# Performance work log

Measured on AMD Instinct MI355X. Metric: run time of the kernel, lower is better.

## Reference

```python
import jax, jax.numpy as jnp
import numpy as np

KERNELS = ("gaussian", "laplacian", "gaussian", "laplacian")
N, M, D, N_PER = 384, 384, 64, 200


def setup_inputs():
    key = jax.random.key(0)
    kx, ky, kb, kp = jax.random.split(key, 4)
    X = jax.random.normal(kx, (N, D), dtype=jnp.float32)
    Y = jax.random.normal(ky, (M, D), dtype=jnp.float32)
    # positive bandwidths of realistic magnitude for d=64 gaussian/laplacian kernels
    bandwidths = jax.random.uniform(kb, (4,), dtype=jnp.float32) * 8.0 + 4.0
    # each row is a random permutation of n+m indices (torch.randperm equivalent)
    perms = jax.vmap(lambda k: jax.random.permutation(k, N + M))(
        jax.random.split(kp, N_PER)).astype(jnp.int32)
    return {"X": X, "Y": Y, "bandwidths": bandwidths, "perms": perms}


def _pairwise_dist(Z):
    # torch.cdist(Z, Z, p=2); eps keeps sqrt grad finite on the zero diagonal
    sq = jnp.sum(Z * Z, axis=1)
    d2 = jnp.maximum(sq[:, None] + sq[None, :] - 2.0 * (Z @ Z.T), 0.0)
    return jnp.sqrt(d2 + 1e-12)


def reference(X, Y, bandwidths, perms):
    n, m = X.shape[0], Y.shape[0]
    Z = jnp.concatenate([X, Y], axis=0)            # [n+m, d]
    dist = _pairwise_dist(Z)                        # [n+m, n+m]
    idx = jnp.arange(min(n, m))
    perm_X, perm_Y = perms[:, :n], perms[:, n:]    # [n_per, n], [n_per, m]
    U, U_b = [], []
    for i, kern in enumerate(KERNELS):
        b = bandwidths[i]
        if kern == "gaussian":
            K = jnp.exp(-(dist * dist) / (b * b))
        else:  # laplacian
            K = jnp.exp(-dist / b)
        # mmd_u's in-place K_XY[diag]=0 mutates the view of K, so zero first
        K = K.at[idx, n + idx].set(0.0)
        K_XX, K_YY, K_XY = K[:n, :n], K[n:, n:], K[:n, n:]
        mmd = ((K_XX.sum() - jnp.trace(K_XX)) / (n * (n - 1))
               + (K_YY.sum() - jnp.trace(K_YY)) / (m * (m - 1))
               - 2.0 * K_XY.sum() / (n * m))
        U.append(mmd)
        # fast_perm: gather permuted blocks, zero diagonals, reduce per permutation
        diagK = jnp.diagonal(K)
        sXX = K[perm_X[:, :, None], perm_X[:, None, :]].sum((1, 2)) - diagK[perm_X].sum(1)
        sYY = K[perm_Y[:, :, None], perm_Y[:, None, :]].sum((1, 2)) - diagK[perm_Y].sum(1)
        sXY = (K[perm_X[:, :, None], perm_Y[:, None, :]].sum((1, 2))
               - K[perm_X[:, idx], perm_Y[:, idx]].sum(1))
        U_b.append(sXX / (n * (n - 1)) + sYY / (m * (m - 1)) - 2.0 * sXY / (n * m))
    U = jnp.stack(U)[:, None]    # [n_b, 1]  == compute_U_stats U.unsqueeze(1)
    U_b = jnp.stack(U_b)         # [n_b, n_per]
    return jnp.concatenate([U, U_b], axis=1)  # [n_b, 1 + n_per]
```

## Files before the change

kernel.cpp:

```cpp
#include <hip/hip_runtime.h>

#define NTOT 768
#define NHALF 384
#define DDIM 64
#define NPER 200
#define PPAD 256
#define NKER 4
#define CHUNK 192
#define NMB 12
#define NNC 8

typedef __attribute__((ext_vector_type(8))) short short8;
typedef __attribute__((ext_vector_type(4))) float floatx4;

constexpr int K0SZ  = NTOT * NTOT;
constexpr int OF_KH = 0;
constexpr int KH_FLOATS = NKER * K0SZ / 2;
constexpr int OF_RS0 = OF_KH + KH_FLOATS;
constexpr int OF_RSX = OF_RS0 + NKER * NTOT;
constexpr int OF_RSY = OF_RSX + NKER * NTOT;
constexpr int OF_C   = OF_RSY + NKER * NTOT;
constexpr int OF_ROWM = OF_C + NKER * NHALF;
constexpr int OF_COLM = OF_ROWM + NKER * NTOT;
constexpr int OF_SCAL = OF_COLM + NKER * NTOT;
constexpr int OF_STT  = OF_SCAL + 16;
constexpr int STT_FLOATS = PPAD * NTOT / 2;
constexpr int OF_Q0P  = OF_STT + STT_FLOATS;

__device__ __forceinline__ unsigned short f2bf(float f) {
    unsigned int u = __float_as_uint(f);
    return (unsigned short)((u + 0x7FFFu + ((u >> 16) & 1u)) >> 16);
}
__device__ __forceinline__ float bf2f(unsigned short h) {
    return __uint_as_float(((unsigned int)h) << 16);
}

__global__ __launch_bounds__(256) void k_stage1(const float* __restrict__ X,
                                                const float* __restrict__ Y,
                                                const float* __restrict__ bw,
                                                const int* __restrict__ perms,
                                                float* __restrict__ ws) {
    __shared__ float zb[CHUNK * 65];
    __shared__ float zaS[DDIM];
    __shared__ float redw[32];
    int bid = blockIdx.x, tid = threadIdx.x;
    unsigned short* STT = (unsigned short*)(ws + OF_STT);

    if (bid < NPER) {
        if (tid < 192) {
            ((uint2*)(STT + bid * NTOT))[tid] = make_uint2(0u, 0u);
            if (bid < PPAD - NPER)
                ((uint2*)(STT + (NPER + bid) * NTOT))[tid] = make_uint2(0u, 0u);
        }
        __syncthreads();
        int v = perms[bid * NTOT + tid];
        STT[bid * NTOT + v] = 0x3F80;
        if (tid < NHALF - 256) {
            int v2 = perms[bid * NTOT + 256 + tid];
            STT[bid * NTOT + v2] = 0x3F80;
        }
        return;
    }

    int a = bid - NPER;
    unsigned short* KH = (unsigned short*)(ws + OF_KH);
    const float* za = (a < NHALF) ? X + a * DDIM : Y + (a - NHALF) * DDIM;
    if (tid < DDIM) zaS[tid] = za[tid];
    float ib2[NKER], ib1[NKER];
#pragma unroll
    for (int k = 0; k < NKER; ++k) { float b = bw[k]; ib2[k] = 1.f / (b * b); ib1[k] = 1.f / b; }
    __syncthreads();
    float sqa = 0.f;
#pragma unroll
    for (int d = 0; d < DDIM; ++d) sqa = fmaf(zaS[d], zaS[d], sqa);

    float accX[NKER] = {0.f, 0.f, 0.f, 0.f};
    float accY[NKER] = {0.f, 0.f, 0.f, 0.f};

    for (int c0 = 0; c0 < NTOT; c0 += CHUNK) {
        __syncthreads();
        for (int idx = tid; idx < CHUNK * DDIM; idx += 256) {
            int r = idx >> 6, d = idx & 63;
            int gr = c0 + r;
            const float* zr = (gr < NHALF) ? X + gr * DDIM : Y + (gr - NHALF) * DDIM;
            zb[r * 65 + d] = zr[d];
        }
        __syncthreads();
        if (tid < CHUNK) {
            int b = c0 + tid;
            float dot = 0.f, sqb = 0.f;
#pragma unroll
            for (int d = 0; d < DDIM; ++d) {
                float zv = zb[tid * 65 + d];
                dot = fmaf(zaS[d], zv, dot);
                sqb = fmaf(zv, zv, sqb);
            }
            float d2 = (sqa + sqb) - 2.f * dot;
            if (b == a) d2 = 0.f;
            d2 = fmaxf(d2, 0.f);
            float d2e = d2 + 1e-12f;
            float dist = sqrtf(d2e);
#pragma unroll
            for (int k = 0; k < NKER; ++k) {
                float val = ((k & 1) == 0) ? __expf(-d2e * ib2[k]) : __expf(-dist * ib1[k]);
                KH[k * K0SZ + a * NTOT + b] = f2bf(val);
                if (b < NHALF) accX[k] += val; else accY[k] += val;
                if (a < NHALF && b == a + NHALF) ws[OF_C + k * NHALF + a] = val;
            }
        }
    }
    float vals[8];
#pragma unroll
    for (int k = 0; k < NKER; ++k) { vals[k] = accX[k]; vals[4 + k] = accY[k]; }
#pragma unroll
    for (int off = 32; off > 0; off >>= 1)
#pragma unroll
        for (int v = 0; v < 8; ++v) vals[v] += __shfl_down(vals[v], off, 64);
    int wid = tid >> 6, lane = tid & 63;
    if (lane == 0)
#pragma unroll
        for (int v = 0; v < 8; ++v) redw[wid * 8 + v] = vals[v];
    __syncthreads();
    if (tid == 0) {
#pragma unroll
        for (int k = 0; k < NKER; ++k) {
            float sx = redw[k] + redw[8 + k] + redw[16 + k] + redw[24 + k];
            float sy = redw[4 + k] + redw[12 + k] + redw[20 + k] + redw[28 + k];
            ws[OF_RS0 + k * NTOT + a] = sx + sy;
            ws[OF_RSX + k * NTOT + a] = sx;
            ws[OF_RSY + k * NTOT + a] = sy;
        }
    }
}

__global__ __launch_bounds__(256) void k_stage2(const float* __restrict__ bw,
                                                float* __restrict__ ws,
                                                float* __restrict__ out) {
    __shared__ float shred[128];
    int bid = blockIdx.x, tid = threadIdx.x;

    if (bid < NMB * NNC * NKER) {
        int mb = bid % NMB;
        int t  = bid / NMB;
        int nc = t % NNC;
        int k  = t / NNC;
        int wave = tid >> 6, lane = tid & 63;
        int m0 = mb * 64 + wave * 16;
        int n0 = nc * 32;
        int row = lane & 15, quad = lane >> 4;
        const unsigned short* KH  = (const unsigned short*)(ws + OF_KH);
        const unsigned short* STT = (const unsigned short*)(ws + OF_STT);
        const unsigned short* aptr = KH + k * K0SZ + (m0 + row) * NTOT + quad * 8;
        const unsigned short* b0p  = STT + (n0 + row) * NTOT + quad * 8;
        const unsigned short* b1p  = STT + (n0 + 16 + row) * NTOT + quad * 8;
        floatx4 acc00 = {0.f,0.f,0.f,0.f}, acc01 = {0.f,0.f,0.f,0.f};
        floatx4 acc10 = {0.f,0.f,0.f,0.f}, acc11 = {0.f,0.f,0.f,0.f};
        for (int kk = 0; kk < NTOT; kk += 64) {
            short8 a0  = *(const short8*)(aptr + kk);
            short8 a1  = *(const short8*)(aptr + kk + 32);
            short8 b00 = *(const short8*)(b0p + kk);
            short8 b01 = *(const short8*)(b0p + kk + 32);
            short8 b10 = *(const short8*)(b1p + kk);
            short8 b11 = *(const short8*)(b1p + kk + 32);
            acc00 = __builtin_amdgcn_mfma_f32_16x16x32_bf16(a0, b00, acc00, 0, 0, 0);
            acc01 = __builtin_amdgcn_mfma_f32_16x16x32_bf16(a1, b01, acc01, 0, 0, 0);
            acc10 = __builtin_amdgcn_mfma_f32_16x16x32_bf16(a0, b10, acc10, 0, 0, 0);
            acc11 = __builtin_amdgcn_mfma_f32_16x16x32_bf16(a1, b11, acc11, 0, 0, 0);
        }
        const unsigned short* s0 = STT + (n0 + row) * NTOT + m0 + quad * 4;
        const unsigned short* s1 = STT + (n0 + 16 + row) * NTOT + m0 + quad * 4;
        float p0 = 0.f, p1 = 0.f;
#pragma unroll
        for (int r = 0; r < 4; ++r) {
            p0 += (acc00[r] + acc01[r]) * bf2f(s0[r]);
            p1 += (acc10[r] + acc11[r]) * bf2f(s1[r]);
        }
        p0 += __shfl_down(p0, 32, 64); p0 += __shfl_down(p0, 16, 64);
        p1 += __shfl_down(p1, 32, 64); p1 += __shfl_down(p1, 16, 64);
        if (lane < 16) { shred[wave * 32 + lane] = p0; shred[wave * 32 + 16 + lane] = p1; }
        __syncthreads();
        if (tid < 32) {
            float s = shred[tid] + shred[32 + tid] + shred[64 + tid] + shred[96 + tid];
            ws[OF_Q0P + (k * NMB + mb) * PPAD + n0 + tid] = s;
        }
        return;
    }

    int k = bid - NMB * NNC * NKER;
    float v[5] = {0.f, 0.f, 0.f, 0.f, 0.f};
    for (int a = tid; a < NTOT; a += 256) v[0] += ws[OF_RS0 + k * NTOT + a];
    for (int a = tid; a < NHALF; a += 256) {
        v[1] += ws[OF_C + k * NHALF + a];
        v[2] += ws[OF_RSX + k * NTOT + a];
        v[3] += ws[OF_RSY + k * NTOT + NHALF + a];
        v[4] += ws[OF_RSY + k * NTOT + a];
    }
#pragma unroll
    for (int off = 32; off > 0; off >>= 1)
#pragma unroll
        for (int j = 0; j < 5; ++j) v[j] += __shfl_down(v[j], off, 64);
    int wid = tid >> 6, lane = tid & 63;
    if (lane == 0)
#pragma unroll
        for (int j = 0; j < 5; ++j) shred[wid * 8 + j] = v[j];
    __syncthreads();
    if (tid == 0) {
        float tot0 = shred[0] + shred[8] + shred[16] + shred[24];
        float csum = shred[1] + shred[9] + shred[17] + shred[25];
        float sxx  = shred[2] + shred[10] + shred[18] + shred[26];
        float syy  = shred[3] + shred[11] + shred[19] + shred[27];
        float sxy  = shred[4] + shred[12] + shred[20] + shred[28];
        float b = bw[k];
        float dist0 = sqrtf(1e-12f);
        float dk = ((k & 1) == 0) ? expf(-(dist0 * dist0) / (b * b)) : expf(-dist0 / b);
        ws[OF_SCAL + k * 4 + 0] = tot0 - csum;
        ws[OF_SCAL + k * 4 + 1] = dk;
        double U = ((double)sxx - 384.0 * (double)dk) * (1.0 / 147072.0)
                 + ((double)syy - 384.0 * (double)dk) * (1.0 / 147072.0)
                 - 2.0 * ((double)sxy - (double)csum) * (1.0 / 147456.0);
        out[k * 201] = (float)U;
    }
    for (int idx = tid; idx < NTOT; idx += 256) {
        float r0 = ws[OF_RS0 + k * NTOT + idx];
        float cx = (idx < NHALF)  ? ws[OF_C + k * NHALF + idx] : 0.f;
        float cy = (idx >= NHALF) ? ws[OF_C + k * NHALF + idx - NHALF] : 0.f;
        ws[OF_ROWM + k * NTOT + idx] = r0 - cx;
        ws[OF_COLM + k * NTOT + idx] = r0 - cy;
    }
}

__global__ __launch_bounds__(384) void k_perm(const int* __restrict__ perms,
                                              const float* __restrict__ ws,
                                              float* __restrict__ out) {
    int p = blockIdx.x, i = threadIdx.x;
    const unsigned short* STT = (const unsigned short*)(ws + OF_STT);
    const unsigned short* KH  = (const unsigned short*)(ws + OF_KH);
    int a  = perms[p * NTOT + i];
    int bY = perms[p * NTOT + NHALF + i];
    float si  = bf2f(STT[p * NTOT + i]);
    float si2 = bf2f(STT[p * NTOT + NHALF + i]);
    float v[16];
#pragma unroll
    for (int k = 0; k < NKER; ++k) {
        v[k * 4 + 0] = ws[OF_ROWM + k * NTOT + a];
        v[k * 4 + 1] = ws[OF_COLM + k * NTOT + a];
        float kv = bf2f(KH[k * K0SZ + a * NTOT + bY]);
        if (a < NHALF && bY == a + NHALF) kv = 0.f;
        v[k * 4 + 2] = kv;
        v[k * 4 + 3] = ws[OF_C + k * NHALF + i] * si * si2;
    }
#pragma unroll
    for (int off = 32; off > 0; off >>= 1)
#pragma unroll
        for (int j = 0; j < 16; ++j) v[j] += __shfl_down(v[j], off, 64);
    __shared__ float redw[6 * 16];
    int wid = i >> 6, lane = i & 63;
    if (lane == 0)
#pragma unroll
        for (int j = 0; j < 16; ++j) redw[wid * 16 + j] = v[j];
    __syncthreads();
    if (i < 16) {
        float s = 0.f;
#pragma unroll
        for (int w = 0; w < 6; ++w) s += redw[w * 16 + i];
        redw[i] = s;
    }
    __syncthreads();
    if (i < NKER) {
        int k = i;
        double rs = redw[k * 4 + 0], cs = redw[k * 4 + 1];
        double pair = redw[k * 4 + 2], qc = redw[k * 4 + 3];
        double total_mod = (double)ws[OF_SCAL + k * 4 + 0];
        double dk        = (double)ws[OF_SCAL + k * 4 + 1];
        double q = -qc;
#pragma unroll
        for (int mb = 0; mb < NMB; ++mb) q += (double)ws[OF_Q0P + (k * NMB + mb) * PPAD + p];
        double sXX = q - 384.0 * dk;
        double sYY = total_mod - rs - cs + q - 384.0 * dk;
        double sXY = rs - q - pair;
        out[k * 201 + 1 + p] =
            (float)(sXX * (1.0 / 147072.0) + sYY * (1.0 / 147072.0) - 2.0 * sXY * (1.0 / 147456.0));
    }
}

extern "C" void kernel_launch(void* const* d_in, const int* in_sizes, int n_in,
                              void* d_out, int out_size, void* d_ws, size_t ws_size,
                              hipStream_t stream) {
    const float* X     = (const float*)d_in[0];
    const float* Y     = (const float*)d_in[1];
    const float* bw    = (const float*)d_in[2];
    const int*   perms = (const int*)d_in[3];
    float* ws  = (float*)d_ws;
    float* out = (float*)d_out;

    k_stage1<<<NPER + NTOT, 256, 0, stream>>>(X, Y, bw, perms, ws);
    k_stage2<<<NMB * NNC * NKER + NKER, 256, 0, stream>>>(bw, ws, out);
    k_perm  <<<NPER, 384, 0, stream>>>(perms, ws, out);
}
```

Baseline: 107.1 us.

## Fuse three stages into one cooperative persistent kernel with grid syncs

Merges the three launches (distance/kernel matrix build, bf16 MFMA permutation GEMM, per-permutation reduction) into one cooperative kernel of 256 blocks that loops over work units and uses grid.sync between phases. The GEMM phase also now computes 64 permutation columns per block instead of 32, halving its block count and reusing each loaded A fragment across four B tiles. Phase C now uses 256 threads with a strided loop. The aim is to remove inter-kernel launch gaps and get more reuse in the GEMM. The cost is that only 256 blocks do the 968 phase-A units, and grid-wide barriers are added. A fallback to three separate launches remains if the cooperative launch fails.

```diff
diff --git a/kernel.cpp b/kernel.cpp
--- a/kernel.cpp
+++ b/kernel.cpp
@@ -1,4 +1,7 @@
 #include <hip/hip_runtime.h>
+#include <hip/hip_cooperative_groups.h>
+
+namespace cg = cooperative_groups;
 
 #define NTOT 768
 #define NHALF 384
@@ -8,7 +11,9 @@
 #define NKER 4
 #define CHUNK 192
 #define NMB 12
-#define NNC 8
+#define NBLK 256
+#define NB_GEMM 192
+#define NA_UNITS (NPER + NTOT)
 
 typedef __attribute__((ext_vector_type(8))) short short8;
 typedef __attribute__((ext_vector_type(4))) float floatx4;
@@ -27,6 +32,8 @@
 constexpr int STT_FLOATS = PPAD * NTOT / 2;
 constexpr int OF_Q0P  = OF_STT + STT_FLOATS;
 
+constexpr int SMEMF = CHUNK * 65 + DDIM + 32;
+
 __device__ __forceinline__ unsigned short f2bf(float f) {
     unsigned int u = __float_as_uint(f);
     return (unsigned short)((u + 0x7FFFu + ((u >> 16) & 1u)) >> 16);
@@ -35,45 +42,42 @@
     return __uint_as_float(((unsigned int)h) << 16);
 }
 
-__global__ __launch_bounds__(256) void k_stage1(const float* __restrict__ X,
-                                                const float* __restrict__ Y,
-                                                const float* __restrict__ bw,
-                                                const int* __restrict__ perms,
-                                                float* __restrict__ ws) {
-    __shared__ float zb[CHUNK * 65];
-    __shared__ float zaS[DDIM];
-    __shared__ float redw[32];
-    int bid = blockIdx.x, tid = threadIdx.x;
+__device__ __forceinline__ void phaseA_unit(int u, const float* __restrict__ X,
+                                            const float* __restrict__ Y,
+                                            const int* __restrict__ perms,
+                                            const float* ib2, const float* ib1,
+                                            float* __restrict__ ws, float* smem) {
+    int tid = threadIdx.x, wave = tid >> 6, lane = tid & 63;
+    float* zb  = smem;
+    float* zaS = smem + CHUNK * 65;
+    float* redw = smem + CHUNK * 65 + DDIM;
     unsigned short* STT = (unsigned short*)(ws + OF_STT);
-
-    if (bid < NPER) {
+    unsigned short* KH  = (unsigned short*)(ws + OF_KH);
+    __syncthreads();
+
+    if (u < NPER) {
         if (tid < 192) {
-            ((uint2*)(STT + bid * NTOT))[tid] = make_uint2(0u, 0u);
-            if (bid < PPAD - NPER)
-                ((uint2*)(STT + (NPER + bid) * NTOT))[tid] = make_uint2(0u, 0u);
+            ((uint2*)(STT + u * NTOT))[tid] = make_uint2(0u, 0u);
+            if (u < PPAD - NPER)
+                ((uint2*)(STT + (NPER + u) * NTOT))[tid] = make_uint2(0u, 0u);
         }
         __syncthreads();
-        int v = perms[bid * NTOT + tid];
-        STT[bid * NTOT + v] = 0x3F80;
+        int v = perms[u * NTOT + tid];
+        STT[u * NTOT + v] = 0x3F80;
         if (tid < NHALF - 256) {
-            int v2 = perms[bid * NTOT + 256 + tid];
-            STT[bid * NTOT + v2] = 0x3F80;
+            int v2 = perms[u * NTOT + 256 + tid];
+            STT[u * NTOT + v2] = 0x3F80;
         }
         return;
     }
 
-    int a = bid - NPER;
-    unsigned short* KH = (unsigned short*)(ws + OF_KH);
+    int a = u - NPER;
     const float* za = (a < NHALF) ? X + a * DDIM : Y + (a - NHALF) * DDIM;
     if (tid < DDIM) zaS[tid] = za[tid];
-    float ib2[NKER], ib1[NKER];
-#pragma unroll
-    for (int k = 0; k < NKER; ++k) { float b = bw[k]; ib2[k] = 1.f / (b * b); ib1[k] = 1.f / b; }
     __syncthreads();
     float sqa = 0.f;
 #pragma unroll
     for (int d = 0; d < DDIM; ++d) sqa = fmaf(zaS[d], zaS[d], sqa);
-
     float accX[NKER] = {0.f, 0.f, 0.f, 0.f};
     float accY[NKER] = {0.f, 0.f, 0.f, 0.f};
 
@@ -116,10 +120,10 @@
     for (int off = 32; off > 0; off >>= 1)
 #pragma unroll
         for (int v = 0; v < 8; ++v) vals[v] += __shfl_down(vals[v], off, 64);
-    int wid = tid >> 6, lane = tid & 63;
+    __syncthreads();
     if (lane == 0)
 #pragma unroll
-        for (int v = 0; v < 8; ++v) redw[wid * 8 + v] = vals[v];
+        for (int v = 0; v < 8; ++v) redw[wave * 8 + v] = vals[v];
     __syncthreads();
     if (tid == 0) {
 #pragma unroll
@@ -133,60 +137,57 @@
     }
 }
 
-__global__ __launch_bounds__(256) void k_stage2(const float* __restrict__ bw,
-                                                float* __restrict__ ws,
-                                                float* __restrict__ out) {
-    __shared__ float shred[128];
-    int bid = blockIdx.x, tid = threadIdx.x;
-
-    if (bid < NMB * NNC * NKER) {
-        int mb = bid % NMB;
-        int t  = bid / NMB;
-        int nc = t % NNC;
-        int k  = t / NNC;
-        int wave = tid >> 6, lane = tid & 63;
-        int m0 = mb * 64 + wave * 16;
-        int n0 = nc * 32;
-        int row = lane & 15, quad = lane >> 4;
-        const unsigned short* KH  = (const unsigned short*)(ws + OF_KH);
-        const unsigned short* STT = (const unsigned short*)(ws + OF_STT);
-        const unsigned short* aptr = KH + k * K0SZ + (m0 + row) * NTOT + quad * 8;
-        const unsigned short* b0p  = STT + (n0 + row) * NTOT + quad * 8;
-        const unsigned short* b1p  = STT + (n0 + 16 + row) * NTOT + quad * 8;
-        floatx4 acc00 = {0.f,0.f,0.f,0.f}, acc01 = {0.f,0.f,0.f,0.f};
-        floatx4 acc10 = {0.f,0.f,0.f,0.f}, acc11 = {0.f,0.f,0.f,0.f};
-        for (int kk = 0; kk < NTOT; kk += 64) {
-            short8 a0  = *(const short8*)(aptr + kk);
-            short8 a1  = *(const short8*)(aptr + kk + 32);
-            short8 b00 = *(const short8*)(b0p + kk);
-            short8 b01 = *(const short8*)(b0p + kk + 32);
-            short8 b10 = *(const short8*)(b1p + kk);
-            short8 b11 = *(const short8*)(b1p + kk + 32);
-            acc00 = __builtin_amdgcn_mfma_f32_16x16x32_bf16(a0, b00, acc00, 0, 0, 0);
-            acc01 = __builtin_amdgcn_mfma_f32_16x16x32_bf16(a1, b01, acc01, 0, 0, 0);
-            acc10 = __builtin_amdgcn_mfma_f32_16x16x32_bf16(a0, b10, acc10, 0, 0, 0);
-            acc11 = __builtin_amdgcn_mfma_f32_16x16x32_bf16(a1, b11, acc11, 0, 0, 0);
-        }
-        const unsigned short* s0 = STT + (n0 + row) * NTOT + m0 + quad * 4;
-        const unsigned short* s1 = STT + (n0 + 16 + row) * NTOT + m0 + quad * 4;
-        float p0 = 0.f, p1 = 0.f;
-#pragma unroll
-        for (int r = 0; r < 4; ++r) {
-            p0 += (acc00[r] + acc01[r]) * bf2f(s0[r]);
-            p1 += (acc10[r] + acc11[r]) * bf2f(s1[r]);
-        }
-        p0 += __shfl_down(p0, 32, 64); p0 += __shfl_down(p0, 16, 64);
-        p1 += __shfl_down(p1, 32, 64); p1 += __shfl_down(p1, 16, 64);
-        if (lane < 16) { shred[wave * 32 + lane] = p0; shred[wave * 32 + 16 + lane] = p1; }
-        __syncthreads();
-        if (tid < 32) {
-            float s = shred[tid] + shred[32 + tid] + shred[64 + tid] + shred[96 + tid];
-            ws[OF_Q0P + (k * NMB + mb) * PPAD + n0 + tid] = s;
-        }
-        return;
-    }
-
-    int k = bid - NMB * NNC * NKER;
+__device__ __forceinline__ void phaseB_gemm(int unit, float* __restrict__ ws, float* smem) {
+    int tid = threadIdx.x, wave = tid >> 6, lane = tid & 63;
+    int mb = unit % NMB;
+    int t  = unit / NMB;
+    int nc = t & 3;
+    int k  = t >> 2;
+    int m0 = mb * 64 + wave * 16;
+    int n0 = nc * 64;
+    int row = lane & 15, quad = lane >> 4;
+    const unsigned short* KH  = (const unsigned short*)(ws + OF_KH);
+    const unsigned short* STT = (const unsigned short*)(ws + OF_STT);
+    const unsigned short* aptr = KH + k * K0SZ + (m0 + row) * NTOT + quad * 8;
+    floatx4 acc[4][2];
+#pragma unroll
+    for (int j = 0; j < 4; ++j)
+#pragma unroll
+        for (int h = 0; h < 2; ++h) acc[j][h] = (floatx4){0.f, 0.f, 0.f, 0.f};
+    for (int kk = 0; kk < NTOT; kk += 64) {
+        short8 a0 = *(const short8*)(aptr + kk);
+        short8 a1 = *(const short8*)(aptr + kk + 32);
+#pragma unroll
+        for (int j = 0; j < 4; ++j) {
+            const unsigned short* bp = STT + (n0 + j * 16 + row) * NTOT + quad * 8 + kk;
+            short8 b0 = *(const short8*)(bp);
+            short8 b1 = *(const short8*)(bp + 32);
+            acc[j][0] = __builtin_amdgcn_mfma_f32_16x16x32_bf16(a0, b0, acc[j][0], 0, 0, 0);
+            acc[j][1] = __builtin_amdgcn_mfma_f32_16x16x32_bf16(a1, b1, acc[j][1], 0, 0, 0);
+        }
+    }
+    __syncthreads();
+#pragma unroll
+    for (int j = 0; j < 4; ++j) {
+        const unsigned short* sp = STT + (n0 + j * 16 + row) * NTOT + m0 + quad * 4;
+        float p = 0.f;
+#pragma unroll
+        for (int r = 0; r < 4; ++r) p += (acc[j][0][r] + acc[j][1][r]) * bf2f(sp[r]);
+        p += __shfl_down(p, 32, 64);
+        p += __shfl_down(p, 16, 64);
+        if (lane < 16) smem[wave * 64 + j * 16 + lane] = p;
+    }
+    __syncthreads();
+    if (tid < 64) {
+        float s = smem[tid] + smem[64 + tid] + smem[128 + tid] + smem[192 + tid];
+        ws[OF_Q0P + (k * NMB + mb) * PPAD + n0 + tid] = s;
+    }
+}
+
+__device__ __forceinline__ void phaseB_final(int k, const float* __restrict__ bw,
+                                             float* __restrict__ ws, float* __restrict__ out,
+                                             float* smem) {
+    int tid = threadIdx.x, wave = tid >> 6, lane = tid & 63;
     float v[5] = {0.f, 0.f, 0.f, 0.f, 0.f};
     for (int a = tid; a < NTOT; a += 256) v[0] += ws[OF_RS0 + k * NTOT + a];
     for (int a = tid; a < NHALF; a += 256) {
@@ -199,17 +200,17 @@
     for (int off = 32; off > 0; off >>= 1)
 #pragma unroll
         for (int j = 0; j < 5; ++j) v[j] += __shfl_down(v[j], off, 64);
-    int wid = tid >> 6, lane = tid & 63;
+    __syncthreads();
     if (lane == 0)
 #pragma unroll
-        for (int j = 0; j < 5; ++j) shred[wid * 8 + j] = v[j];
+        for (int j = 0; j < 5; ++j) smem[wave * 8 + j] = v[j];
     __syncthreads();
     if (tid == 0) {
-        float tot0 = shred[0] + shred[8] + shred[16] + shred[24];
-        float csum = shred[1] + shred[9] + shred[17] + shred[25];
-        float sxx  = shred[2] + shred[10] + shred[18] + shred[26];
-        float syy  = shred[3] + shred[11] + shred[19] + shred[27];
-        float sxy  = shred[4] + shred[12] + shred[20] + shred[28];
+        float tot0 = smem[0] + smem[8] + smem[16] + smem[24];
+        float csum = smem[1] + smem[9] + smem[17] + smem[25];
+        float sxx  = smem[2] + smem[10] + smem[18] + smem[26];
+        float syy  = smem[3] + smem[11] + smem[19] + smem[27];
+        float sxy  = smem[4] + smem[12] + smem[20] + smem[28];
         float b = bw[k];
         float dist0 = sqrtf(1e-12f);
         float dk = ((k & 1) == 0) ? expf(-(dist0 * dist0) / (b * b)) : expf(-dist0 / b);
@@ -229,47 +230,43 @@
     }
 }
 
-__global__ __launch_bounds__(384) void k_perm(const int* __restrict__ perms,
-                                              const float* __restrict__ ws,
-                                              float* __restrict__ out) {
-    int p = blockIdx.x, i = threadIdx.x;
+__device__ __forceinline__ void phaseC_unit(int p, const int* __restrict__ perms,
+                                            const float* __restrict__ ws,
+                                            float* __restrict__ out, float* smem) {
+    int tid = threadIdx.x, wave = tid >> 6, lane = tid & 63;
     const unsigned short* STT = (const unsigned short*)(ws + OF_STT);
     const unsigned short* KH  = (const unsigned short*)(ws + OF_KH);
-    int a  = perms[p * NTOT + i];
-    int bY = perms[p * NTOT + NHALF + i];
-    float si  = bf2f(STT[p * NTOT + i]);
-    float si2 = bf2f(STT[p * NTOT + NHALF + i]);
-    float v[16];
-#pragma unroll
-    for (int k = 0; k < NKER; ++k) {
-        v[k * 4 + 0] = ws[OF_ROWM + k * NTOT + a];
-        v[k * 4 + 1] = ws[OF_COLM + k * NTOT + a];
-        float kv = bf2f(KH[k * K0SZ + a * NTOT + bY]);
-        if (a < NHALF && bY == a + NHALF) kv = 0.f;
-        v[k * 4 + 2] = kv;
-        v[k * 4 + 3] = ws[OF_C + k * NHALF + i] * si * si2;
+    float v[16] = {0.f};
+    for (int i = tid; i < NHALF; i += 256) {
+        int a  = perms[p * NTOT + i];
+        int bY = perms[p * NTOT + NHALF + i];
+        float si  = bf2f(STT[p * NTOT + i]);
+        float si2 = bf2f(STT[p * NTOT + NHALF + i]);
+#pragma unroll
+        for (int k = 0; k < NKER; ++k) {
+            v[k * 4 + 0] += ws[OF_ROWM + k * NTOT + a];
+            v[k * 4 + 1] += ws[OF_COLM + k * NTOT + a];
+            float kv = bf2f(KH[k * K0SZ + a * NTOT + bY]);
+            if (a < NHALF && bY == a + NHALF) kv = 0.f;
+            v[k * 4 + 2] += kv;
+            v[k * 4 + 3] += ws[OF_C + k * NHALF + i] * si * si2;
+        }
     }
 #pragma unroll
     for (int off = 32; off > 0; off >>= 1)
 #pragma unroll
         for (int j = 0; j < 16; ++j) v[j] += __shfl_down(v[j], off, 64);
-    __shared__ float redw[6 * 16];
-    int wid = i >> 6, lane = i & 63;
+    __syncthreads();
     if (lane == 0)
 #pragma unroll
-        for (int j = 0; j < 16; ++j) redw[wid * 16 + j] = v[j];
-    __syncthreads();
-    if (i < 16) {
-        float s = 0.f;
-#pragma unroll
-        for (int w = 0; w < 6; ++w) s += redw[w * 16 + i];
-        redw[i] = s;
-    }
-    __syncthreads();
-    if (i < NKER) {
-        int k = i;
-        double rs = redw[k * 4 + 0], cs = redw[k * 4 + 1];
-        double pair = redw[k * 4 + 2], qc = redw[k * 4 + 3];
+        for (int j = 0; j < 16; ++j) smem[wave * 16 + j] = v[j];
+    __syncthreads();
+    if (tid < 16) smem[64 + tid] = smem[tid] + smem[16 + tid] + smem[32 + tid] + smem[48 + tid];
+    __syncthreads();
+    if (tid < NKER) {
+        int k = tid;
+        double rs = smem[64 + k * 4 + 0], cs = smem[64 + k * 4 + 1];
+        double pair = smem[64 + k * 4 + 2], qc = smem[64 + k * 4 + 3];
         double total_mod = (double)ws[OF_SCAL + k * 4 + 0];
         double dk        = (double)ws[OF_SCAL + k * 4 + 1];
         double q = -qc;
@@ -281,6 +278,59 @@
         out[k * 201 + 1 + p] =
             (float)(sXX * (1.0 / 147072.0) + sYY * (1.0 / 147072.0) - 2.0 * sXY * (1.0 / 147456.0));
     }
+}
+
+__global__ __launch_bounds__(256) void k_mega(const float* __restrict__ X,
+                                              const float* __restrict__ Y,
+                                              const float* __restrict__ bw,
+                                              const int* __restrict__ perms,
+                                              float* __restrict__ ws,
+                                              float* __restrict__ out) {
+    __shared__ float smem[SMEMF];
+    cg::grid_group grid = cg::this_grid();
+    float ib2[NKER], ib1[NKER];
+#pragma unroll
+    for (int k = 0; k < NKER; ++k) { float b = bw[k]; ib2[k] = 1.f / (b * b); ib1[k] = 1.f / b; }
+
+    for (int u = blockIdx.x; u < NA_UNITS; u += NBLK)
+        phaseA_unit(u, X, Y, perms, ib2, ib1, ws, smem);
+
+    __threadfence();
+    grid.sync();
+
+    if (blockIdx.x < NB_GEMM)           phaseB_gemm(blockIdx.x, ws, smem);
+    else if (blockIdx.x < NB_GEMM + NKER) phaseB_final(blockIdx.x - NB_GEMM, bw, ws, out, smem);
+
+    __threadfence();
+    grid.sync();
+
+    if (blockIdx.x < NPER) phaseC_unit(blockIdx.x, perms, ws, out, smem);
+}
+
+__global__ __launch_bounds__(256) void k_s1(const float* __restrict__ X,
+                                            const float* __restrict__ Y,
+                                            const float* __restrict__ bw,
+                                            const int* __restrict__ perms,
+                                            float* __restrict__ ws) {
+    __shared__ float smem[SMEMF];
+    float ib2[NKER], ib1[NKER];
+#pragma unroll
+    for (int k = 0; k < NKER; ++k) { float b = bw[k]; ib2[k] = 1.f / (b * b); ib1[k] = 1.f / b; }
+    phaseA_unit(blockIdx.x, X, Y, perms, ib2, ib1, ws, smem);
+}
+
+__global__ __launch_bounds__(256) void k_s2(const float* __restrict__ bw,
+                                            float* __restrict__ ws, float* __restrict__ out) {
+    __shared__ float smem[256];
+    if (blockIdx.x < NB_GEMM) phaseB_gemm(blockIdx.x, ws, smem);
+    else                      phaseB_final(blockIdx.x - NB_GEMM, bw, ws, out, smem);
+}
+
+__global__ __launch_bounds__(256) void k_s3(const int* __restrict__ perms,
+                                            const float* __restrict__ ws,
+                                            float* __restrict__ out) {
+    __shared__ float smem[128];
+    phaseC_unit(blockIdx.x, perms, ws, out, smem);
 }
 
 extern "C" void kernel_launch(void* const* d_in, const int* in_sizes, int n_in,
@@ -293,7 +343,12 @@
     float* ws  = (float*)d_ws;
     float* out = (float*)d_out;
 
-    k_stage1<<<NPER + NTOT, 256, 0, stream>>>(X, Y, bw, perms, ws);
-    k_stage2<<<NMB * NNC * NKER + NKER, 256, 0, stream>>>(bw, ws, out);
-    k_perm  <<<NPER, 384, 0, stream>>>(perms, ws, out);
-}
+    void* args[] = {(void*)&X, (void*)&Y, (void*)&bw, (void*)&perms, (void*)&ws, (void*)&out};
+    hipError_t e = hipLaunchCooperativeKernel((void*)k_mega, dim3(NBLK), dim3(256), args, 0, stream);
+    if (e != hipSuccess) {
+        (void)hipGetLastError();
+        k_s1<<<NA_UNITS, 256, 0, stream>>>(X, Y, bw, perms, ws);
+        k_s2<<<NB_GEMM + NKER, 256, 0, stream>>>(bw, ws, out);
+        k_s3<<<NPER, 256, 0, stream>>>(perms, ws, out);
+    }
+}
```

Result: slower. 283.8 us (+165.0%).
